# Optimization experiments

Hardware: AMD Instinct MI355X
Metric: run time of the kernel (lower is better)

The kernel has to match this reference:

```python
import jax, jax.numpy as jnp
import numpy as np

N = 50000   # nodes
E = 600000  # edges
D = 128     # input_dim
H = 128     # hidden_dim
K = 2       # num_layers (propagation hops)


def setup_inputs() -> dict:
    key = jax.random.key(0)
    k1, k2, k3 = jax.random.split(key, 3)
    x = jax.random.normal(k1, (N, D), dtype=jnp.float32)
    edge_index = jax.random.randint(k2, (2, E), 0, N, dtype=jnp.int64)
    # Linear(input_dim -> hidden_dim) params (PyG default: glorot-ish weight, zero bias)
    W = jax.random.normal(k3, (H, D), dtype=jnp.float32) / np.float32(np.sqrt(D))
    b = jnp.zeros((H,), dtype=jnp.float32)
    return {"x": x, "edge_index": edge_index, "W": W, "b": b}


def reference(x, edge_index, W, b):
    n = x.shape[0]
    loop = jnp.arange(n, dtype=edge_index.dtype)
    # gcn_norm: add self-loops with weight 1, symmetric normalization
    row = jnp.concatenate([edge_index[0], loop])  # source nodes
    col = jnp.concatenate([edge_index[1], loop])  # target nodes
    w = jnp.ones(row.shape[0], dtype=x.dtype)
    deg = jax.ops.segment_sum(w, col, num_segments=n)
    dinv = jnp.where(deg > 0, jax.lax.rsqrt(deg), jnp.zeros_like(deg))
    norm = dinv[row] * w * dinv[col]  # [E+N]
    # K hops of normalized sparse propagation: x <- A_hat @ x
    for _ in range(K):
        x = jax.ops.segment_sum(norm[:, None] * x[row], col, num_segments=n)
    # Linear projection + activation
    z = x @ W.T + b
    return jax.nn.relu(z)
```

## Files before the change

### kernel.cpp

```cpp
#include <hip/hip_runtime.h>

#define D 128
#define CAP 128
typedef unsigned int uint;
typedef unsigned short ushort;
typedef __attribute__((ext_vector_type(8))) short bf16x8;
typedef __attribute__((ext_vector_type(4))) float f32x4;

__device__ __forceinline__ float2 bf2_to_f2(uint v) {
    union { uint u; float f; } a, b;
    a.u = v << 16;
    b.u = v & 0xffff0000u;
    return make_float2(a.f, b.f);
}
__device__ __forceinline__ uint f2_to_bf2(float x, float y) {
    uint xu = __float_as_uint(x), yu = __float_as_uint(y);
    xu += 0x7fffu + ((xu >> 16) & 1u);
    yu += 0x7fffu + ((yu >> 16) & 1u);
    return (xu >> 16) | (yu & 0xffff0000u);
}

__global__ __launch_bounds__(256) void build_cast_kernel(
        const int* __restrict__ ei, int E, int* __restrict__ deg, int* __restrict__ slots,
        const float* __restrict__ x, uint2* __restrict__ zX, int n,
        const float* __restrict__ W, uint* __restrict__ Wbf,
        int cntB, int xB) {
    int b = blockIdx.x, t = threadIdx.x;
    if (b < cntB) {
        int e = b * 256 + t;
        if (e < E) {
            int r = ei[e];
            int c = ei[E + e];
            int pos = atomicAdd(&deg[c], 1);
            if (pos < CAP) slots[c * CAP + pos] = r;
        }
    } else if (b < cntB + xB) {
        int idx = (b - cntB) * 256 + t;
        if (idx < n * 32) {
            float4 v = ((const float4*)x)[idx];
            uint2 o;
            o.x = f2_to_bf2(v.x, v.y);
            o.y = f2_to_bf2(v.z, v.w);
            zX[idx] = o;
        }
    } else {
        int i = (b - cntB - xB) * 256 + t;
        if (i < (D * D) / 2) {
            float2 wv = ((const float2*)W)[i];
            Wbf[i] = f2_to_bf2(wv.x, wv.y);
        }
    }
}

__global__ __launch_bounds__(256) void prop1_kernel(const uint* __restrict__ zin,
                                                    uint* __restrict__ zout,
                                                    const int* __restrict__ deg,
                                                    const int* __restrict__ slots,
                                                    int n) {
    int wv = threadIdx.x >> 6, lane = threadIdx.x & 63;
    int c = blockIdx.x * 4 + wv;
    if (c >= n) return;
    int len = deg[c]; if (len > CAP) len = CAP;
    const int* lst = slots + c * CAP;
    size_t selfoff = (size_t)c * 64 + lane;
    float dc = rsqrtf((float)(len + 1));
    float2 sf = bf2_to_f2(zin[selfoff]);
    float2 acc = make_float2(sf.x * dc, sf.y * dc);
    int k = 0;
    for (; k + 7 < len; k += 8) {
        int r0 = lst[k],     r1 = lst[k + 1], r2 = lst[k + 2], r3 = lst[k + 3];
        int r4 = lst[k + 4], r5 = lst[k + 5], r6 = lst[k + 6], r7 = lst[k + 7];
        uint v0 = zin[(size_t)r0 * 64 + lane], v1 = zin[(size_t)r1 * 64 + lane];
        uint v2 = zin[(size_t)r2 * 64 + lane], v3 = zin[(size_t)r3 * 64 + lane];
        uint v4 = zin[(size_t)r4 * 64 + lane], v5 = zin[(size_t)r5 * 64 + lane];
        uint v6 = zin[(size_t)r6 * 64 + lane], v7 = zin[(size_t)r7 * 64 + lane];
        float d0 = rsqrtf((float)(deg[r0] + 1)), d1 = rsqrtf((float)(deg[r1] + 1));
        float d2 = rsqrtf((float)(deg[r2] + 1)), d3 = rsqrtf((float)(deg[r3] + 1));
        float d4 = rsqrtf((float)(deg[r4] + 1)), d5 = rsqrtf((float)(deg[r5] + 1));
        float d6 = rsqrtf((float)(deg[r6] + 1)), d7 = rsqrtf((float)(deg[r7] + 1));
        float2 f0 = bf2_to_f2(v0), f1 = bf2_to_f2(v1), f2 = bf2_to_f2(v2), f3 = bf2_to_f2(v3);
        float2 f4 = bf2_to_f2(v4), f5 = bf2_to_f2(v5), f6 = bf2_to_f2(v6), f7 = bf2_to_f2(v7);
        acc.x += (fmaf(d0, f0.x, d1 * f1.x) + fmaf(d2, f2.x, d3 * f3.x))
               + (fmaf(d4, f4.x, d5 * f5.x) + fmaf(d6, f6.x, d7 * f7.x));
        acc.y += (fmaf(d0, f0.y, d1 * f1.y) + fmaf(d2, f2.y, d3 * f3.y))
               + (fmaf(d4, f4.y, d5 * f5.y) + fmaf(d6, f6.y, d7 * f7.y));
    }
    for (; k < len; ++k) {
        int r = lst[k];
        float d = rsqrtf((float)(deg[r] + 1));
        float2 f = bf2_to_f2(zin[(size_t)r * 64 + lane]);
        acc.x = fmaf(d, f.x, acc.x);
        acc.y = fmaf(d, f.y, acc.y);
    }
    float sc = dc * dc;
    zout[selfoff] = f2_to_bf2(acc.x * sc, acc.y * sc);
}

__global__ __launch_bounds__(256) void prop2_kernel(const uint* __restrict__ zin,
                                                    uint* __restrict__ zout,
                                                    const int* __restrict__ deg,
                                                    const int* __restrict__ slots,
                                                    int n) {
    int wv = threadIdx.x >> 6, lane = threadIdx.x & 63;
    int c = blockIdx.x * 4 + wv;
    if (c >= n) return;
    int len = deg[c]; if (len > CAP) len = CAP;
    const int* lst = slots + c * CAP;
    size_t selfoff = (size_t)c * 64 + lane;
    float2 acc = bf2_to_f2(zin[selfoff]);
    int k = 0;
    for (; k + 7 < len; k += 8) {
        int r0 = lst[k],     r1 = lst[k + 1], r2 = lst[k + 2], r3 = lst[k + 3];
        int r4 = lst[k + 4], r5 = lst[k + 5], r6 = lst[k + 6], r7 = lst[k + 7];
        uint v0 = zin[(size_t)r0 * 64 + lane], v1 = zin[(size_t)r1 * 64 + lane];
        uint v2 = zin[(size_t)r2 * 64 + lane], v3 = zin[(size_t)r3 * 64 + lane];
        uint v4 = zin[(size_t)r4 * 64 + lane], v5 = zin[(size_t)r5 * 64 + lane];
        uint v6 = zin[(size_t)r6 * 64 + lane], v7 = zin[(size_t)r7 * 64 + lane];
        float2 f0 = bf2_to_f2(v0), f1 = bf2_to_f2(v1), f2 = bf2_to_f2(v2), f3 = bf2_to_f2(v3);
        float2 f4 = bf2_to_f2(v4), f5 = bf2_to_f2(v5), f6 = bf2_to_f2(v6), f7 = bf2_to_f2(v7);
        acc.x += ((f0.x + f1.x) + (f2.x + f3.x)) + ((f4.x + f5.x) + (f6.x + f7.x));
        acc.y += ((f0.y + f1.y) + (f2.y + f3.y)) + ((f4.y + f5.y) + (f6.y + f7.y));
    }
    for (; k < len; ++k) {
        float2 f = bf2_to_f2(zin[(size_t)lst[k] * 64 + lane]);
        acc.x += f.x; acc.y += f.y;
    }
    float s = rsqrtf((float)(len + 1));
    zout[selfoff] = f2_to_bf2(acc.x * s, acc.y * s);
}

#define GN 64
__global__ __launch_bounds__(256) void gemm_mfma(const uint4* __restrict__ x2,
                                                 const uint4* __restrict__ Wbf,
                                                 const float* __restrict__ bias,
                                                 float* __restrict__ out, int n) {
    __shared__ __align__(16) ushort xs[GN][136];
    __shared__ __align__(16) ushort ws[D][136];
    int t = threadIdx.x;
    int n0 = blockIdx.x * GN;
    for (int i = t; i < D * 16; i += 256) {
        int row = i >> 4, c8 = i & 15;
        uint4 v = Wbf[i];
        *(uint4*)&ws[row][c8 * 8] = v;
    }
    for (int i = t; i < GN * 16; i += 256) {
        int row = i >> 4, c8 = i & 15;
        int node = n0 + row;
        uint4 v = (node < n) ? x2[(size_t)node * 16 + c8] : make_uint4(0u, 0u, 0u, 0u);
        *(uint4*)&xs[row][c8 * 8] = v;
    }
    __syncthreads();

    int w = t >> 6, lane = t & 63;
    int m0 = w * 16;
    int mrow = lane & 15, quad = lane >> 4;

    bf16x8 a[4];
#pragma unroll
    for (int q = 0; q < 4; ++q)
        a[q] = *(const bf16x8*)&xs[m0 + mrow][q * 32 + quad * 8];

    f32x4 acc[8];
#pragma unroll
    for (int ht = 0; ht < 8; ++ht) {
        acc[ht] = (f32x4){0.f, 0.f, 0.f, 0.f};
#pragma unroll
        for (int q = 0; q < 4; ++q) {
            bf16x8 bfr = *(const bf16x8*)&ws[ht * 16 + mrow][q * 32 + quad * 8];
            acc[ht] = __builtin_amdgcn_mfma_f32_16x16x32_bf16(a[q], bfr, acc[ht], 0, 0, 0);
        }
    }

#pragma unroll
    for (int ht = 0; ht < 8; ++ht) {
        int h = ht * 16 + mrow;
        float bv = bias[h];
#pragma unroll
        for (int reg = 0; reg < 4; ++reg) {
            int node = n0 + m0 + quad * 4 + reg;
            if (node < n)
                out[(size_t)node * D + h] = fmaxf(acc[ht][reg] + bv, 0.f);
        }
    }
}

extern "C" void kernel_launch(void* const* d_in, const int* in_sizes, int n_in,
                              void* d_out, int out_size, void* d_ws, size_t ws_size,
                              hipStream_t stream) {
    const float* x  = (const float*)d_in[0];
    const int*   ei = (const int*)d_in[1];
    const float* W  = (const float*)d_in[2];
    const float* bias = (const float*)d_in[3];
    float* out = (float*)d_out;
    int N = in_sizes[0] / D;
    int E = in_sizes[1] / 2;

    char* p = (char*)d_ws;
    auto alloc = [&](size_t bytes) -> void* {
        void* r = p; p += (bytes + 511) & ~(size_t)511; return r;
    };
    int*    deg     = (int*)alloc((size_t)N * 4);
    int*    slots   = (int*)alloc((size_t)N * CAP * 4);
    uint*   zX      = (uint*)alloc((size_t)N * 64 * 4);
    uint*   zB      = (uint*)alloc((size_t)N * 64 * 4);
    uint*   zA      = (uint*)alloc((size_t)N * 64 * 4);
    uint*   Wbf     = (uint*)alloc((size_t)(D * D / 2) * 4);

    int cntB = (E + 255) / 256;
    int xB   = (N * 32 + 255) / 256;
    int wB   = ((D * D / 2) + 255) / 256;

    hipMemsetAsync(deg, 0, (size_t)N * 4, stream);
    build_cast_kernel<<<cntB + xB + wB, 256, 0, stream>>>(ei, E, deg, slots, x, (uint2*)zX, N,
                                                          W, Wbf, cntB, xB);
    prop1_kernel<<<(N + 3) / 4, 256, 0, stream>>>(zX, zB, deg, slots, N);
    prop2_kernel<<<(N + 3) / 4, 256, 0, stream>>>(zB, zA, deg, slots, N);
    gemm_mfma<<<(N + GN - 1) / GN, 256, 0, stream>>>((const uint4*)zA, (const uint4*)Wbf, bias, out, N);
}
```

Before: 201.6 us.

## Prescale input by source degree and partition edge build by target range

After: 180.0 us. 10.7% less time.

```diff
diff --git a/kernel.cpp b/kernel.cpp
--- a/kernel.cpp
+++ b/kernel.cpp
@@ -2,6 +2,7 @@
 
 #define D 128
 #define CAP 128
+#define NR 8
 typedef unsigned int uint;
 typedef unsigned short ushort;
 typedef __attribute__((ext_vector_type(8))) short bf16x8;
@@ -20,31 +21,26 @@
     return (xu >> 16) | (yu & 0xffff0000u);
 }
 
-__global__ __launch_bounds__(256) void build_cast_kernel(
-        const int* __restrict__ ei, int E, int* __restrict__ deg, int* __restrict__ slots,
-        const float* __restrict__ x, uint2* __restrict__ zX, int n,
-        const float* __restrict__ W, uint* __restrict__ Wbf,
-        int cntB, int xB) {
+__global__ __launch_bounds__(256) void edge_build_kernel(
+        const int* __restrict__ ei, int E, int n,
+        int* __restrict__ deg, int* __restrict__ slots,
+        const float* __restrict__ W, uint* __restrict__ Wbf, int edgeB) {
     int b = blockIdx.x, t = threadIdx.x;
-    if (b < cntB) {
-        int e = b * 256 + t;
+    if (b < edgeB) {
+        int range = b & (NR - 1);
+        int e = (b >> 3) * 256 + t;
         if (e < E) {
-            int r = ei[e];
             int c = ei[E + e];
-            int pos = atomicAdd(&deg[c], 1);
-            if (pos < CAP) slots[c * CAP + pos] = r;
-        }
-    } else if (b < cntB + xB) {
-        int idx = (b - cntB) * 256 + t;
-        if (idx < n * 32) {
-            float4 v = ((const float4*)x)[idx];
-            uint2 o;
-            o.x = f2_to_bf2(v.x, v.y);
-            o.y = f2_to_bf2(v.z, v.w);
-            zX[idx] = o;
+            int per = (n + NR - 1) / NR;
+            int lo = range * per;
+            if (c >= lo && c < lo + per) {
+                int r = ei[e];
+                int pos = atomicAdd(&deg[c], 1);
+                if (pos < CAP) slots[(size_t)c * CAP + pos] = r;
+            }
         }
     } else {
-        int i = (b - cntB - xB) * 256 + t;
+        int i = (b - edgeB) * 256 + t;
         if (i < (D * D) / 2) {
             float2 wv = ((const float2*)W)[i];
             Wbf[i] = f2_to_bf2(wv.x, wv.y);
@@ -52,60 +48,32 @@
     }
 }
 
-__global__ __launch_bounds__(256) void prop1_kernel(const uint* __restrict__ zin,
-                                                    uint* __restrict__ zout,
-                                                    const int* __restrict__ deg,
-                                                    const int* __restrict__ slots,
-                                                    int n) {
+__global__ __launch_bounds__(256) void scale_cast_kernel(
+        const float* __restrict__ x, const int* __restrict__ deg,
+        uint2* __restrict__ zX, int n) {
+    int idx = blockIdx.x * 256 + threadIdx.x;
+    if (idx < n * 32) {
+        int node = idx >> 5;
+        float dv = rsqrtf((float)(deg[node] + 1));
+        float4 v = ((const float4*)x)[idx];
+        uint2 o;
+        o.x = f2_to_bf2(v.x * dv, v.y * dv);
+        o.y = f2_to_bf2(v.z * dv, v.w * dv);
+        zX[idx] = o;
+    }
+}
+
+template<bool HOP1>
+__global__ __launch_bounds__(256) void prop_kernel(const uint* __restrict__ zin,
+                                                   uint* __restrict__ zout,
+                                                   const int* __restrict__ deg,
+                                                   const int* __restrict__ slots,
+                                                   int n) {
     int wv = threadIdx.x >> 6, lane = threadIdx.x & 63;
     int c = blockIdx.x * 4 + wv;
     if (c >= n) return;
     int len = deg[c]; if (len > CAP) len = CAP;
-    const int* lst = slots + c * CAP;
-    size_t selfoff = (size_t)c * 64 + lane;
-    float dc = rsqrtf((float)(len + 1));
-    float2 sf = bf2_to_f2(zin[selfoff]);
-    float2 acc = make_float2(sf.x * dc, sf.y * dc);
-    int k = 0;
-    for (; k + 7 < len; k += 8) {
-        int r0 = lst[k],     r1 = lst[k + 1], r2 = lst[k + 2], r3 = lst[k + 3];
-        int r4 = lst[k + 4], r5 = lst[k + 5], r6 = lst[k + 6], r7 = lst[k + 7];
-        uint v0 = zin[(size_t)r0 * 64 + lane], v1 = zin[(size_t)r1 * 64 + lane];
-        uint v2 = zin[(size_t)r2 * 64 + lane], v3 = zin[(size_t)r3 * 64 + lane];
-        uint v4 = zin[(size_t)r4 * 64 + lane], v5 = zin[(size_t)r5 * 64 + lane];
-        uint v6 = zin[(size_t)r6 * 64 + lane], v7 = zin[(size_t)r7 * 64 + lane];
-        float d0 = rsqrtf((float)(deg[r0] + 1)), d1 = rsqrtf((float)(deg[r1] + 1));
-        float d2 = rsqrtf((float)(deg[r2] + 1)), d3 = rsqrtf((float)(deg[r3] + 1));
-        float d4 = rsqrtf((float)(deg[r4] + 1)), d5 = rsqrtf((float)(deg[r5] + 1));
-        float d6 = rsqrtf((float)(deg[r6] + 1)), d7 = rsqrtf((float)(deg[r7] + 1));
-        float2 f0 = bf2_to_f2(v0), f1 = bf2_to_f2(v1), f2 = bf2_to_f2(v2), f3 = bf2_to_f2(v3);
-        float2 f4 = bf2_to_f2(v4), f5 = bf2_to_f2(v5), f6 = bf2_to_f2(v6), f7 = bf2_to_f2(v7);
-        acc.x += (fmaf(d0, f0.x, d1 * f1.x) + fmaf(d2, f2.x, d3 * f3.x))
-               + (fmaf(d4, f4.x, d5 * f5.x) + fmaf(d6, f6.x, d7 * f7.x));
-        acc.y += (fmaf(d0, f0.y, d1 * f1.y) + fmaf(d2, f2.y, d3 * f3.y))
-               + (fmaf(d4, f4.y, d5 * f5.y) + fmaf(d6, f6.y, d7 * f7.y));
-    }
-    for (; k < len; ++k) {
-        int r = lst[k];
-        float d = rsqrtf((float)(deg[r] + 1));
-        float2 f = bf2_to_f2(zin[(size_t)r * 64 + lane]);
-        acc.x = fmaf(d, f.x, acc.x);
-        acc.y = fmaf(d, f.y, acc.y);
-    }
-    float sc = dc * dc;
-    zout[selfoff] = f2_to_bf2(acc.x * sc, acc.y * sc);
-}
-
-__global__ __launch_bounds__(256) void prop2_kernel(const uint* __restrict__ zin,
-                                                    uint* __restrict__ zout,
-                                                    const int* __restrict__ deg,
-                                                    const int* __restrict__ slots,
-                                                    int n) {
-    int wv = threadIdx.x >> 6, lane = threadIdx.x & 63;
-    int c = blockIdx.x * 4 + wv;
-    if (c >= n) return;
-    int len = deg[c]; if (len > CAP) len = CAP;
-    const int* lst = slots + c * CAP;
+    const int* lst = slots + (size_t)c * CAP;
     size_t selfoff = (size_t)c * 64 + lane;
     float2 acc = bf2_to_f2(zin[selfoff]);
     int k = 0;
@@ -121,12 +89,30 @@
         acc.x += ((f0.x + f1.x) + (f2.x + f3.x)) + ((f4.x + f5.x) + (f6.x + f7.x));
         acc.y += ((f0.y + f1.y) + (f2.y + f3.y)) + ((f4.y + f5.y) + (f6.y + f7.y));
     }
-    for (; k < len; ++k) {
+    if (k + 3 < len) {
+        int r0 = lst[k], r1 = lst[k + 1], r2 = lst[k + 2], r3 = lst[k + 3];
+        uint v0 = zin[(size_t)r0 * 64 + lane], v1 = zin[(size_t)r1 * 64 + lane];
+        uint v2 = zin[(size_t)r2 * 64 + lane], v3 = zin[(size_t)r3 * 64 + lane];
+        float2 f0 = bf2_to_f2(v0), f1 = bf2_to_f2(v1), f2 = bf2_to_f2(v2), f3 = bf2_to_f2(v3);
+        acc.x += (f0.x + f1.x) + (f2.x + f3.x);
+        acc.y += (f0.y + f1.y) + (f2.y + f3.y);
+        k += 4;
+    }
+    if (k + 1 < len) {
+        int r0 = lst[k], r1 = lst[k + 1];
+        uint v0 = zin[(size_t)r0 * 64 + lane], v1 = zin[(size_t)r1 * 64 + lane];
+        float2 f0 = bf2_to_f2(v0), f1 = bf2_to_f2(v1);
+        acc.x += f0.x + f1.x;
+        acc.y += f0.y + f1.y;
+        k += 2;
+    }
+    if (k < len) {
         float2 f = bf2_to_f2(zin[(size_t)lst[k] * 64 + lane]);
         acc.x += f.x; acc.y += f.y;
     }
     float s = rsqrtf((float)(len + 1));
-    zout[selfoff] = f2_to_bf2(acc.x * s, acc.y * s);
+    float sc = HOP1 ? s * s : s;
+    zout[selfoff] = f2_to_bf2(acc.x * sc, acc.y * sc);
 }
 
 #define GN 64
@@ -206,14 +192,14 @@
     uint*   zA      = (uint*)alloc((size_t)N * 64 * 4);
     uint*   Wbf     = (uint*)alloc((size_t)(D * D / 2) * 4);
 
-    int cntB = (E + 255) / 256;
-    int xB   = (N * 32 + 255) / 256;
-    int wB   = ((D * D / 2) + 255) / 256;
+    int edgeB = ((E + 255) / 256) * NR;
+    int wB    = ((D * D / 2) + 255) / 256;
+    int xB    = (N * 32 + 255) / 256;
 
     hipMemsetAsync(deg, 0, (size_t)N * 4, stream);
-    build_cast_kernel<<<cntB + xB + wB, 256, 0, stream>>>(ei, E, deg, slots, x, (uint2*)zX, N,
-                                                          W, Wbf, cntB, xB);
-    prop1_kernel<<<(N + 3) / 4, 256, 0, stream>>>(zX, zB, deg, slots, N);
-    prop2_kernel<<<(N + 3) / 4, 256, 0, stream>>>(zB, zA, deg, slots, N);
+    edge_build_kernel<<<edgeB + wB, 256, 0, stream>>>(ei, E, N, deg, slots, W, Wbf, edgeB);
+    scale_cast_kernel<<<xB, 256, 0, stream>>>(x, deg, (uint2*)zX, N);
+    prop_kernel<true ><<<(N + 3) / 4, 256, 0, stream>>>(zX, zB, deg, slots, N);
+    prop_kernel<false><<<(N + 3) / 4, 256, 0, stream>>>(zB, zA, deg, slots, N);
     gemm_mfma<<<(N + GN - 1) / GN, 256, 0, stream>>>((const uint4*)zA, (const uint4*)Wbf, bias, out, N);
 }
```
